# Kernel tuning notes

Measured on AMD Instinct MI355X. Metric: run time of the kernel, lower is better.

The kernel has to match this reference:

```python
import jax, jax.numpy as jnp
import numpy as np

VOC, TOPIC, EMB, BATCH = 128000, 512, 1024, 1024

def setup_inputs() -> dict:
    key = jax.random.key(0)
    k1, k2, k3 = jax.random.split(key, 3)
    x = jax.random.normal(k1, (TOPIC, BATCH), dtype=jnp.float32)
    beta0 = jax.random.normal(k2, (VOC, EMB), dtype=jnp.float32)
    beta_t = jax.random.normal(k3, (TOPIC, EMB), dtype=jnp.float32) * 0.02  # nn.init.normal_(std=0.02)
    return {"x": x, "beta0": beta0, "beta_t": beta_t, "t": 0}

def reference(x, beta0, beta_t, t):
    # w: [voc, topic] = beta0 [voc, emb] @ beta_t.T [emb, topic]
    # (the t==0 branch and else branch are identical in the source)
    w = jnp.einsum('ve,te->vt', beta0, beta_t)
    w = jax.nn.softmax(w, axis=0)  # softmax over vocab dim (dim=0)
    # out: [voc, batch]
    return jnp.einsum('vt,tb->vb', w, x)
```

## Files before the change

kernel.cpp:

```cpp
#include <hip/hip_runtime.h>

typedef _Float16 f16x8 __attribute__((ext_vector_type(8)));
typedef float    f32x4 __attribute__((ext_vector_type(4)));
typedef unsigned short u16;

#define VOC   128000
#define TOPIC 512
#define EMB   1024
#define BATCH 1024
#define ROWB  128

__device__ __forceinline__ int swz(int row, int kbyte) {
    return row * ROWB + (kbyte ^ ((row & 7) << 4));
}
__device__ __forceinline__ int xcd_swz(int bid, int nwg) {
    return (bid & 7) * (nwg >> 3) + (bid >> 3);
}
union H2U { _Float16 h; u16 u; };

#define SBAR() asm volatile("s_barrier" ::: "memory")
#define WVM0() asm volatile("s_waitcnt vmcnt(0)" ::: "memory")
#define WLG0() asm volatile("s_waitcnt lgkmcnt(0)" ::: "memory")

__global__ void cvt_betat_kernel(const float* __restrict__ betat, u16* __restrict__ bt16) {
    const size_t g = (size_t)blockIdx.x * 256 + threadIdx.x;
    const float4* src = reinterpret_cast<const float4*>(betat) + g * 2;
    float4 a = src[0], b = src[1];
    f16x8 h;
    h[0]=(_Float16)a.x; h[1]=(_Float16)a.y; h[2]=(_Float16)a.z; h[3]=(_Float16)a.w;
    h[4]=(_Float16)b.x; h[5]=(_Float16)b.y; h[6]=(_Float16)b.z; h[7]=(_Float16)b.w;
    *(reinterpret_cast<f16x8*>(bt16) + g) = h;
}

__global__ __launch_bounds__(512, 2) void gemm1_kernel(
    const float* __restrict__ beta0, const u16* __restrict__ bt16,
    u16* __restrict__ Eg, size_t TSTR, int RSTR, float* __restrict__ sg)
{
    __shared__ char lds[98304];

    const int tid  = threadIdx.x;
    const int lane = tid & 63;
    const int wid  = tid >> 6;
    const int wr = wid >> 2, wc = wid & 3;
    const int lr = lane & 15, lk = lane >> 4;
    const int srow8  = lane >> 3;
    const int schunk = ((lane & 7) ^ srow8) * 8;

    const int bid  = xcd_swz(blockIdx.x, gridDim.x);
    const int t0   = (bid & 1) * 256;
    const int tile = bid >> 1;
    const int v0   = tile * 128;

    const int arow = tid >> 2;
    const int asp  = (tid & 3) * 2;

    f32x4 acc[4][4] = {};
    float4 rA[4];

    auto loadA = [&](int kt) {
        const float4* g = reinterpret_cast<const float4*>(
            beta0 + (size_t)(v0 + arow) * EMB + kt * 64 + asp * 8);
        rA[0] = g[0]; rA[1] = g[1]; rA[2] = g[2]; rA[3] = g[3];
    };
    auto issueB = [&](int kt, int buf) {
        const u16* bsrc = bt16 + (size_t)(t0 + wid * 8 + srow8) * EMB + kt * 64 + schunk;
        char* dstb = lds + 32768 + buf * 32768;
        #pragma unroll
        for (int p = 0; p < 4; ++p)
            __builtin_amdgcn_global_load_lds(
                (const __attribute__((address_space(1))) unsigned int*)(bsrc + (size_t)p * 64 * EMB),
                (__attribute__((address_space(3))) unsigned int*)(dstb + (p * 64 + wid * 8) * ROWB),
                16, 0, 0);
    };

    issueB(0, 0);
    loadA(0);

    for (int kt = 0; kt < EMB / 64; ++kt) {
        const int cur = kt & 1;
        char* ldsA = lds + cur * 16384;
        char* ldsB = lds + 32768 + cur * 32768;

        SBAR();
        WVM0();
        {
            f16x8 h;
            h[0]=(_Float16)rA[0].x; h[1]=(_Float16)rA[0].y; h[2]=(_Float16)rA[0].z; h[3]=(_Float16)rA[0].w;
            h[4]=(_Float16)rA[1].x; h[5]=(_Float16)rA[1].y; h[6]=(_Float16)rA[1].z; h[7]=(_Float16)rA[1].w;
            *reinterpret_cast<f16x8*>(ldsA + swz(arow, asp * 16)) = h;
            f16x8 h2;
            h2[0]=(_Float16)rA[2].x; h2[1]=(_Float16)rA[2].y; h2[2]=(_Float16)rA[2].z; h2[3]=(_Float16)rA[2].w;
            h2[4]=(_Float16)rA[3].x; h2[5]=(_Float16)rA[3].y; h2[6]=(_Float16)rA[3].z; h2[7]=(_Float16)rA[3].w;
            *reinterpret_cast<f16x8*>(ldsA + swz(arow, (asp + 1) * 16)) = h2;
        }
        if (kt + 1 < EMB / 64) { issueB(kt + 1, cur ^ 1); loadA(kt + 1); }
        WLG0();
        SBAR();
        #pragma unroll
        for (int ks = 0; ks < 2; ++ks) {
            f16x8 af[4], bf[4];
            #pragma unroll
            for (int m = 0; m < 4; ++m)
                af[m] = *reinterpret_cast<const f16x8*>(ldsA + swz(wr * 64 + m * 16 + lr, ks * 64 + lk * 16));
            #pragma unroll
            for (int n = 0; n < 4; ++n)
                bf[n] = *reinterpret_cast<const f16x8*>(ldsB + swz(wc * 64 + n * 16 + lr, ks * 64 + lk * 16));
            #pragma unroll
            for (int m = 0; m < 4; ++m)
                #pragma unroll
                for (int n = 0; n < 4; ++n)
                    acc[m][n] = __builtin_amdgcn_mfma_f32_16x16x32_f16(
                        af[m], bf[n], acc[m][n], 0, 0, 0);
        }
    }

    __syncthreads();
    u16* ldsE = reinterpret_cast<u16*>(lds);
    float csum = 0.f;
    #pragma unroll
    for (int c = 0; c < 2; ++c) {
        if (wr == c) {
            #pragma unroll
            for (int m = 0; m < 4; ++m)
              #pragma unroll
              for (int n = 0; n < 4; ++n)
                #pragma unroll
                for (int r = 0; r < 4; ++r) {
                    const int row = m * 16 + lk * 4 + r;
                    const int col = wc * 64 + n * 16 + lr;
                    H2U cv; cv.h = (_Float16)__expf(acc[m][n][r]);
                    ldsE[row * 264 + col] = cv.u;
                }
        }
        __syncthreads();
        {
            const int row8 = tid >> 3, seg = tid & 7;
            const int4* srcp = reinterpret_cast<const int4*>(&ldsE[row8 * 264 + seg * 32]);
            u16* dst = Eg + tile * TSTR + (size_t)(c * 64 + row8) * RSTR + t0 + seg * 32;
            int4 v0v = srcp[0], v1v = srcp[1], v2v = srcp[2], v3v = srcp[3];
            int4* dp = reinterpret_cast<int4*>(dst);
            dp[0] = v0v; dp[1] = v1v; dp[2] = v2v; dp[3] = v3v;
        }
        if (tid < 256) {
            float s = 0.f;
            for (int r = 0; r < 64; ++r) { H2U cv; cv.u = ldsE[r * 264 + tid]; s += (float)cv.h; }
            csum += s;
        }
        __syncthreads();
    }
    if (tid < 256) atomicAdd(sg + t0 + tid, csum);
}

__global__ void xst_kernel(const float* __restrict__ x, const float* __restrict__ s,
                           u16* __restrict__ xsT)
{
    __shared__ float tile[32][33];
    const int b0 = blockIdx.x * 32, t0 = blockIdx.y * 32;
    const int tx = threadIdx.x, ty = threadIdx.y;
    tile[ty][tx] = x[(size_t)(t0 + ty) * BATCH + b0 + tx];
    __syncthreads();
    const float sc = 65536.0f / s[t0 + tx];
    H2U cv; cv.h = (_Float16)(tile[tx][ty] * sc);
    xsT[(size_t)(b0 + ty) * TOPIC + t0 + tx] = cv.u;
}

__global__ __launch_bounds__(512, 2) void gemm2a_kernel(
    const u16* __restrict__ Eg, size_t TSTR, int RSTR,
    const u16* __restrict__ xsT, float* __restrict__ out, int c0, int nch)
{
    __shared__ char lds[98304];

    const int tid  = threadIdx.x;
    const int lane = tid & 63;
    const int wid  = tid >> 6;
    const int wr = wid >> 2, wc = wid & 3;
    const int lr = lane & 15, lk = lane >> 4;
    const int srow8  = lane >> 3;
    const int schunk = ((lane & 7) ^ srow8) * 8;

    const int bid   = xcd_swz(blockIdx.x, gridDim.x);
    const int tile  = bid / nch;
    const int chunk = bid % nch;
    const int b0    = c0 + chunk * 256;
    const int v0    = tile * 128;
    const u16* Et   = Eg + tile * TSTR;

    f32x4 acc[4][4] = {};

    auto issueAB = [&](int kt, int buf) {
        const int k0 = kt * 64;
        char* dA = lds + buf * 16384;
        char* dB = lds + 32768 + buf * 32768;
        #pragma unroll
        for (int p = 0; p < 2; ++p) {
            const int rbase = p * 64 + wid * 8;
            __builtin_amdgcn_global_load_lds(
                (const __attribute__((address_space(1))) unsigned int*)
                    (Et + (size_t)(rbase + srow8) * RSTR + k0 + schunk),
                (__attribute__((address_space(3))) unsigned int*)(dA + rbase * ROWB),
                16, 0, 0);
        }
        #pragma unroll
        for (int p = 0; p < 4; ++p) {
            const int rbase = p * 64 + wid * 8;
            __builtin_amdgcn_global_load_lds(
                (const __attribute__((address_space(1))) unsigned int*)
                    (xsT + (size_t)(b0 + rbase + srow8) * TOPIC + k0 + schunk),
                (__attribute__((address_space(3))) unsigned int*)(dB + rbase * ROWB),
                16, 0, 0);
        }
    };

    issueAB(0, 0);

    for (int kt = 0; kt < TOPIC / 64; ++kt) {
        const int cur = kt & 1;
        char* ldsA = lds + cur * 16384;
        char* ldsB = lds + 32768 + cur * 32768;

        SBAR();
        WVM0();
        if (kt + 1 < TOPIC / 64) issueAB(kt + 1, cur ^ 1);
        SBAR();
        #pragma unroll
        for (int ks = 0; ks < 2; ++ks) {
            f16x8 af[4], bf[4];
            #pragma unroll
            for (int m = 0; m < 4; ++m)
                af[m] = *reinterpret_cast<const f16x8*>(ldsA + swz(wr * 64 + m * 16 + lr, ks * 64 + lk * 16));
            #pragma unroll
            for (int n = 0; n < 4; ++n)
                bf[n] = *reinterpret_cast<const f16x8*>(ldsB + swz(wc * 64 + n * 16 + lr, ks * 64 + lk * 16));
            #pragma unroll
            for (int m = 0; m < 4; ++m)
                #pragma unroll
                for (int n = 0; n < 4; ++n)
                    acc[m][n] = __builtin_amdgcn_mfma_f32_16x16x32_f16(
                        af[m], bf[n], acc[m][n], 0, 0, 0);
        }
    }

    #pragma unroll
    for (int m = 0; m < 4; ++m)
      #pragma unroll
      for (int n = 0; n < 4; ++n)
        #pragma unroll
        for (int r = 0; r < 4; ++r) {
            const int row = wr * 64 + m * 16 + lk * 4 + r;
            const int col = wc * 64 + n * 16 + lr;
            out[(size_t)(v0 + row) * BATCH + b0 + col] = acc[m][n][r] * 0x1p-16f;
        }
}

__global__ __launch_bounds__(512, 2) void gemm2b_kernel(
    const u16* __restrict__ EgBase,
    const u16* __restrict__ xsT, float* __restrict__ out)
{
    __shared__ char lds[65536];

    const int tid  = threadIdx.x;
    const int lane = tid & 63;
    const int wid  = tid >> 6;
    const int wr = wid >> 2, wc = wid & 3;
    const int lr = lane & 15, lk = lane >> 4;

    const int bid  = xcd_swz(blockIdx.x, gridDim.x);
    const int tile = bid >> 1;
    const int h    = bid & 1;
    const u16* Et  = EgBase + (size_t)tile * 262144;

    f16x8 af[2][16];
    #pragma unroll
    for (int m = 0; m < 2; ++m) {
        const int row = h * 64 + wr * 32 + m * 16 + lr;
        #pragma unroll
        for (int kb = 0; kb < 16; ++kb)
            af[m][kb] = *reinterpret_cast<const f16x8*>(
                Et + (size_t)row * 2048 + kb * 32 + lk * 8);
    }
    WVM0();
    __syncthreads();

    int4 rX[4];
    auto loadX = [&](int kt) {
        const int srow = tid >> 1;
        const int sp   = (tid & 1) * 4;
        const int4* gv = reinterpret_cast<const int4*>(
            xsT + (size_t)srow * TOPIC + kt * 64 + sp * 8);
        rX[0] = gv[0]; rX[1] = gv[1]; rX[2] = gv[2]; rX[3] = gv[3];
    };
    loadX(0);

    f32x4 acc[2][4] = {};
    for (int kt = 0; kt < 8; ++kt) {
        const int cur = kt & 1;
        char* ldsB = lds + cur * 32768;

        SBAR();
        WVM0();
        {
            const int srow = tid >> 1;
            const int sp   = (tid & 1) * 4;
            *reinterpret_cast<int4*>(ldsB + swz(srow, (sp + 0) * 16)) = rX[0];
            *reinterpret_cast<int4*>(ldsB + swz(srow, (sp + 1) * 16)) = rX[1];
            *reinterpret_cast<int4*>(ldsB + swz(srow, (sp + 2) * 16)) = rX[2];
            *reinterpret_cast<int4*>(ldsB + swz(srow, (sp + 3) * 16)) = rX[3];
        }
        if (kt + 1 < 8) loadX(kt + 1);
        WLG0();
        SBAR();
        #pragma unroll
        for (int kk = 0; kk < 2; ++kk) {
            f16x8 bf[4];
            #pragma unroll
            for (int n = 0; n < 4; ++n)
                bf[n] = *reinterpret_cast<const f16x8*>(ldsB + swz(wc * 64 + n * 16 + lr, kk * 64 + lk * 16));
            #pragma unroll
            for (int m = 0; m < 2; ++m)
                #pragma unroll
                for (int n = 0; n < 4; ++n)
                    acc[m][n] = __builtin_amdgcn_mfma_f32_16x16x32_f16(
                        af[m][kt * 2 + kk], bf[n], acc[m][n], 0, 0, 0);
        }
    }

    #pragma unroll
    for (int m = 0; m < 2; ++m)
      #pragma unroll
      for (int n = 0; n < 4; ++n)
        #pragma unroll
        for (int r = 0; r < 4; ++r) {
            const int row = h * 64 + wr * 32 + m * 16 + lk * 4 + r;
            const int col = wc * 64 + n * 16 + lr;
            out[((size_t)tile * 128 + row) * BATCH + col] = acc[m][n][r] * 0x1p-16f;
        }
}

extern "C" void kernel_launch(void* const* d_in, const int* in_sizes, int n_in,
                              void* d_out, int out_size, void* d_ws, size_t ws_size,
                              hipStream_t stream)
{
    const float* x     = (const float*)d_in[0];
    const float* beta0 = (const float*)d_in[1];
    const float* betat = (const float*)d_in[2];
    float* out = (float*)d_out;

    const size_t need_min = 4096 + (size_t)BATCH * TOPIC * 2;
    if (ws_size < need_min) return;
    float* s_g  = (float*)d_ws;
    u16*   buf1 = (u16*)((char*)d_ws + 4096);

    const size_t E_OFF = 4u * 1024u * 1024u;
    const bool big = ws_size >= E_OFF + (size_t)VOC * TOPIC * 2;

    hipMemsetAsync(d_ws, 0, 2048, stream);
    cvt_betat_kernel<<<256, 256, 0, stream>>>(betat, buf1);

    if (big) {
        u16* EgW = (u16*)((char*)d_ws + E_OFF);
        gemm1_kernel<<<2000, 512, 0, stream>>>(beta0, buf1, EgW, (size_t)128 * 512, 512, s_g);
        xst_kernel<<<dim3(BATCH / 32, TOPIC / 32), dim3(32, 32), 0, stream>>>(x, s_g, buf1);
        gemm2a_kernel<<<4000, 512, 0, stream>>>(EgW, (size_t)128 * 512, 512, buf1, out, 0, 4);
    } else {
        u16* EgO = (u16*)d_out;
        gemm1_kernel<<<2000, 512, 0, stream>>>(beta0, buf1, EgO, (size_t)262144, 2048, s_g);
        xst_kernel<<<dim3(BATCH / 32, TOPIC / 32), dim3(32, 32), 0, stream>>>(x, s_g, buf1);
        gemm2a_kernel<<<3000, 512, 0, stream>>>(EgO, (size_t)262144, 2048, buf1, out, 256, 3);
        gemm2b_kernel<<<2000, 512, 0, stream>>>(EgO, buf1, out);
    }
}
```

Baseline: 515.4 us.

## Triple-buffer LDS and prefetch two stages ahead in both GEMM kernels

Both GEMM main loops move from double buffering with a full vmcnt(0) drain each step to a three-slot LDS ring that prefetches two K-steps ahead. A partial s_waitcnt vmcnt(N) waits only for the current stage's loads. In gemm1 the fp32 A operand is held in two alternating register sets, and the loop is unrolled by two through a macro. The aim is to keep more global loads in flight and hide memory latency behind MFMA work. In exchange it uses more LDS (128KB and 144KB per block) and more registers, which could limit occupancy.

```diff
diff --git a/kernel.cpp b/kernel.cpp
--- a/kernel.cpp
+++ b/kernel.cpp
@@ -20,6 +20,8 @@
 
 #define SBAR() asm volatile("s_barrier" ::: "memory")
 #define WVM0() asm volatile("s_waitcnt vmcnt(0)" ::: "memory")
+#define WVM6() asm volatile("s_waitcnt vmcnt(6)" ::: "memory")
+#define WVM8() asm volatile("s_waitcnt vmcnt(8)" ::: "memory")
 #define WLG0() asm volatile("s_waitcnt lgkmcnt(0)" ::: "memory")
 
 __global__ void cvt_betat_kernel(const float* __restrict__ betat, u16* __restrict__ bt16) {
@@ -36,7 +38,7 @@
     const float* __restrict__ beta0, const u16* __restrict__ bt16,
     u16* __restrict__ Eg, size_t TSTR, int RSTR, float* __restrict__ sg)
 {
-    __shared__ char lds[98304];
+    __shared__ char lds[131072];
 
     const int tid  = threadIdx.x;
     const int lane = tid & 63;
@@ -55,16 +57,18 @@
     const int asp  = (tid & 3) * 2;
 
     f32x4 acc[4][4] = {};
-    float4 rA[4];
-
-    auto loadA = [&](int kt) {
-        const float4* g = reinterpret_cast<const float4*>(
-            beta0 + (size_t)(v0 + arow) * EMB + kt * 64 + asp * 8);
-        rA[0] = g[0]; rA[1] = g[1]; rA[2] = g[2]; rA[3] = g[3];
-    };
-    auto issueB = [&](int kt, int buf) {
+    float4 rAa[4], rAb[4];
+
+    const float4* aBase = reinterpret_cast<const float4*>(
+        beta0 + (size_t)(v0 + arow) * EMB);
+
+#define G1_LOADA(RA, kt) { \
+    const float4* gp = aBase + (kt) * 16 + asp * 2; \
+    RA[0] = gp[0]; RA[1] = gp[1]; RA[2] = gp[2]; RA[3] = gp[3]; }
+
+    auto issueB = [&](int kt) {
         const u16* bsrc = bt16 + (size_t)(t0 + wid * 8 + srow8) * EMB + kt * 64 + schunk;
-        char* dstb = lds + 32768 + buf * 32768;
+        char* dstb = lds + 32768 + (kt % 3) * 32768;
         #pragma unroll
         for (int p = 0; p < 4; ++p)
             __builtin_amdgcn_global_load_lds(
@@ -73,45 +77,46 @@
                 16, 0, 0);
     };
 
-    issueB(0, 0);
-    loadA(0);
-
-    for (int kt = 0; kt < EMB / 64; ++kt) {
-        const int cur = kt & 1;
-        char* ldsA = lds + cur * 16384;
-        char* ldsB = lds + 32768 + cur * 32768;
-
-        SBAR();
-        WVM0();
-        {
-            f16x8 h;
-            h[0]=(_Float16)rA[0].x; h[1]=(_Float16)rA[0].y; h[2]=(_Float16)rA[0].z; h[3]=(_Float16)rA[0].w;
-            h[4]=(_Float16)rA[1].x; h[5]=(_Float16)rA[1].y; h[6]=(_Float16)rA[1].z; h[7]=(_Float16)rA[1].w;
-            *reinterpret_cast<f16x8*>(ldsA + swz(arow, asp * 16)) = h;
-            f16x8 h2;
-            h2[0]=(_Float16)rA[2].x; h2[1]=(_Float16)rA[2].y; h2[2]=(_Float16)rA[2].z; h2[3]=(_Float16)rA[2].w;
-            h2[4]=(_Float16)rA[3].x; h2[5]=(_Float16)rA[3].y; h2[6]=(_Float16)rA[3].z; h2[7]=(_Float16)rA[3].w;
-            *reinterpret_cast<f16x8*>(ldsA + swz(arow, (asp + 1) * 16)) = h2;
-        }
-        if (kt + 1 < EMB / 64) { issueB(kt + 1, cur ^ 1); loadA(kt + 1); }
-        WLG0();
-        SBAR();
-        #pragma unroll
-        for (int ks = 0; ks < 2; ++ks) {
-            f16x8 af[4], bf[4];
-            #pragma unroll
-            for (int m = 0; m < 4; ++m)
-                af[m] = *reinterpret_cast<const f16x8*>(ldsA + swz(wr * 64 + m * 16 + lr, ks * 64 + lk * 16));
-            #pragma unroll
-            for (int n = 0; n < 4; ++n)
-                bf[n] = *reinterpret_cast<const f16x8*>(ldsB + swz(wc * 64 + n * 16 + lr, ks * 64 + lk * 16));
-            #pragma unroll
-            for (int m = 0; m < 4; ++m)
-                #pragma unroll
-                for (int n = 0; n < 4; ++n)
-                    acc[m][n] = __builtin_amdgcn_mfma_f32_16x16x32_f16(
-                        af[m], bf[n], acc[m][n], 0, 0, 0);
-        }
+    issueB(0); G1_LOADA(rAa, 0);
+    issueB(1); G1_LOADA(rAb, 1);
+
+#define G1_STEP(kt, RA) { \
+    SBAR();                        \
+    if ((kt) < 15) { WVM8(); } else { WVM0(); }   \
+    char* ldsA = lds + ((kt) & 1) * 16384; \
+    char* ldsB = lds + 32768 + ((kt) % 3) * 32768; \
+    { f16x8 h; \
+      h[0]=(_Float16)RA[0].x; h[1]=(_Float16)RA[0].y; h[2]=(_Float16)RA[0].z; h[3]=(_Float16)RA[0].w; \
+      h[4]=(_Float16)RA[1].x; h[5]=(_Float16)RA[1].y; h[6]=(_Float16)RA[1].z; h[7]=(_Float16)RA[1].w; \
+      *reinterpret_cast<f16x8*>(ldsA + swz(arow, asp * 16)) = h; \
+      f16x8 h2; \
+      h2[0]=(_Float16)RA[2].x; h2[1]=(_Float16)RA[2].y; h2[2]=(_Float16)RA[2].z; h2[3]=(_Float16)RA[2].w; \
+      h2[4]=(_Float16)RA[3].x; h2[5]=(_Float16)RA[3].y; h2[6]=(_Float16)RA[3].z; h2[7]=(_Float16)RA[3].w; \
+      *reinterpret_cast<f16x8*>(ldsA + swz(arow, (asp + 1) * 16)) = h2; } \
+    if ((kt) + 2 < 16) { issueB((kt) + 2); G1_LOADA(RA, (kt) + 2); } \
+    WLG0(); \
+    SBAR();                        \
+    _Pragma("unroll") \
+    for (int ks = 0; ks < 2; ++ks) { \
+        f16x8 af[4], bf[4]; \
+        _Pragma("unroll") \
+        for (int m = 0; m < 4; ++m) \
+            af[m] = *reinterpret_cast<const f16x8*>(ldsA + swz(wr * 64 + m * 16 + lr, ks * 64 + lk * 16)); \
+        _Pragma("unroll") \
+        for (int n = 0; n < 4; ++n) \
+            bf[n] = *reinterpret_cast<const f16x8*>(ldsB + swz(wc * 64 + n * 16 + lr, ks * 64 + lk * 16)); \
+        _Pragma("unroll") \
+        for (int m = 0; m < 4; ++m) \
+            _Pragma("unroll") \
+            for (int n = 0; n < 4; ++n) \
+                acc[m][n] = __builtin_amdgcn_mfma_f32_16x16x32_f16( \
+                    af[m], bf[n], acc[m][n], 0, 0, 0); \
+    } }
+
+    for (int k2 = 0; k2 < 8; ++k2) {
+        const int kt0 = 2 * k2;
+        G1_STEP(kt0,     rAa);
+        G1_STEP(kt0 + 1, rAb);
     }
 
     __syncthreads();
@@ -168,7 +173,7 @@
     const u16* __restrict__ Eg, size_t TSTR, int RSTR,
     const u16* __restrict__ xsT, float* __restrict__ out, int c0, int nch)
 {
-    __shared__ char lds[98304];
+    __shared__ char lds[147456];
 
     const int tid  = threadIdx.x;
     const int lane = tid & 63;
@@ -187,10 +192,10 @@
 
     f32x4 acc[4][4] = {};
 
-    auto issueAB = [&](int kt, int buf) {
+    auto issueAB = [&](int kt) {
         const int k0 = kt * 64;
-        char* dA = lds + buf * 16384;
-        char* dB = lds + 32768 + buf * 32768;
+        char* dA = lds + (kt % 3) * 16384;
+        char* dB = lds + 49152 + (kt % 3) * 32768;
         #pragma unroll
         for (int p = 0; p < 2; ++p) {
             const int rbase = p * 64 + wid * 8;
@@ -211,16 +216,16 @@
         }
     };
 
-    issueAB(0, 0);
+    issueAB(0);
+    issueAB(1);
 
     for (int kt = 0; kt < TOPIC / 64; ++kt) {
-        const int cur = kt & 1;
-        char* ldsA = lds + cur * 16384;
-        char* ldsB = lds + 32768 + cur * 32768;
+        char* ldsA = lds + (kt % 3) * 16384;
+        char* ldsB = lds + 49152 + (kt % 3) * 32768;
 
         SBAR();
-        WVM0();
-        if (kt + 1 < TOPIC / 64) issueAB(kt + 1, cur ^ 1);
+        if (kt < TOPIC / 64 - 1) { WVM6(); } else { WVM0(); }
+        if (kt + 2 < TOPIC / 64) issueAB(kt + 2);
         SBAR();
         #pragma unroll
         for (int ks = 0; ks < 2; ++ks) {
```

Measured after the change: 523.6 us. About the same (+1.6%).

## Use 256x256 tiles with interleaved LDS staging and MFMA phases in both GEMMs

Applied to the files above, without the earlier changes.

Both GEMMs now compute 256x256 output tiles per block (8x4 accumulators per wave) instead of 128x256, using 128KB double-buffered LDS. Each k-step is split into four phases that overlap global loads and LDS staging with MFMA groups, with s_setprio raised around the MFMAs. The workspace/out-buffer dual path and the register-resident gemm2b are dropped: E is always written into the output buffer, and the chunk that would overwrite it runs last. The aim is more operand reuse and fewer global reads per FLOP. The cost is that the larger LDS footprint limits residency to one block per CU, and the XCD swizzle is generalized for grid sizes that are not multiples of 8.

```diff
diff --git a/kernel.cpp b/kernel.cpp
--- a/kernel.cpp
+++ b/kernel.cpp
@@ -14,13 +14,34 @@
     return row * ROWB + (kbyte ^ ((row & 7) << 4));
 }
 __device__ __forceinline__ int xcd_swz(int bid, int nwg) {
-    return (bid & 7) * (nwg >> 3) + (bid >> 3);
+    int x = bid & 7, o = bid >> 3, q = nwg >> 3, r = nwg & 7;
+    return (x < r ? x * (q + 1) : r * (q + 1) + (x - r) * q) + o;
 }
 union H2U { _Float16 h; u16 u; };
 
 #define SBAR() asm volatile("s_barrier" ::: "memory")
 #define WVM0() asm volatile("s_waitcnt vmcnt(0)" ::: "memory")
 #define WLG0() asm volatile("s_waitcnt lgkmcnt(0)" ::: "memory")
+
+#define GLDS(SRC, DST) __builtin_amdgcn_global_load_lds( \
+    (const __attribute__((address_space(1))) unsigned int*)(SRC), \
+    (__attribute__((address_space(3))) unsigned int*)(DST), 16, 0, 0)
+
+#define RD_A(MH, KS) { _Pragma("unroll") \
+    for (int m = 0; m < 4; ++m) \
+        af[m] = *(const f16x8*)(bufA + wr * 16384 + \
+            swz((MH) * 64 + m * 16 + lr, (KS) * 64 + lk * 16)); }
+#define RD_B(KS) { _Pragma("unroll") \
+    for (int n = 0; n < 4; ++n) \
+        bf[n] = *(const f16x8*)(bufB + (wc >> 1) * 16384 + \
+            swz((wc & 1) * 64 + n * 16 + lr, (KS) * 64 + lk * 16)); }
+#define MFMA16(MH) { \
+    __builtin_amdgcn_s_setprio(1); \
+    _Pragma("unroll") for (int m = 0; m < 4; ++m) \
+    _Pragma("unroll") for (int n = 0; n < 4; ++n) \
+        acc[(MH) * 4 + m][n] = __builtin_amdgcn_mfma_f32_16x16x32_f16( \
+            af[m], bf[n], acc[(MH) * 4 + m][n], 0, 0, 0); \
+    __builtin_amdgcn_s_setprio(0); }
 
 __global__ void cvt_betat_kernel(const float* __restrict__ betat, u16* __restrict__ bt16) {
     const size_t g = (size_t)blockIdx.x * 256 + threadIdx.x;
@@ -34,9 +55,9 @@
 
 __global__ __launch_bounds__(512, 2) void gemm1_kernel(
     const float* __restrict__ beta0, const u16* __restrict__ bt16,
-    u16* __restrict__ Eg, size_t TSTR, int RSTR, float* __restrict__ sg)
-{
-    __shared__ char lds[98304];
+    u16* __restrict__ Eg, float* __restrict__ sg)
+{
+    __shared__ char lds[131072];
 
     const int tid  = threadIdx.x;
     const int lane = tid & 63;
@@ -46,80 +67,82 @@
     const int srow8  = lane >> 3;
     const int schunk = ((lane & 7) ^ srow8) * 8;
 
-    const int bid  = xcd_swz(blockIdx.x, gridDim.x);
-    const int t0   = (bid & 1) * 256;
-    const int tile = bid >> 1;
-    const int v0   = tile * 128;
-
-    const int arow = tid >> 2;
-    const int asp  = (tid & 3) * 2;
-
-    f32x4 acc[4][4] = {};
-    float4 rA[4];
-
-    auto loadA = [&](int kt) {
-        const float4* g = reinterpret_cast<const float4*>(
-            beta0 + (size_t)(v0 + arow) * EMB + kt * 64 + asp * 8);
-        rA[0] = g[0]; rA[1] = g[1]; rA[2] = g[2]; rA[3] = g[3];
-    };
-    auto issueB = [&](int kt, int buf) {
-        const u16* bsrc = bt16 + (size_t)(t0 + wid * 8 + srow8) * EMB + kt * 64 + schunk;
-        char* dstb = lds + 32768 + buf * 32768;
-        #pragma unroll
-        for (int p = 0; p < 4; ++p)
-            __builtin_amdgcn_global_load_lds(
-                (const __attribute__((address_space(1))) unsigned int*)(bsrc + (size_t)p * 64 * EMB),
-                (__attribute__((address_space(3))) unsigned int*)(dstb + (p * 64 + wid * 8) * ROWB),
-                16, 0, 0);
-    };
-
-    issueB(0, 0);
-    loadA(0);
-
-    for (int kt = 0; kt < EMB / 64; ++kt) {
-        const int cur = kt & 1;
-        char* ldsA = lds + cur * 16384;
-        char* ldsB = lds + 32768 + cur * 32768;
-
-        SBAR();
+    const int bid   = xcd_swz(blockIdx.x, gridDim.x);
+    const int tile  = bid >> 1;
+    const int chunk = bid & 1;
+    const int v0 = tile * 256, t0 = chunk * 256;
+
+    const int a_row = tid >> 1, a_kh = tid & 1;
+    const float* aRowP = beta0 + (size_t)(v0 + a_row) * EMB + a_kh * 32;
+
+    f32x4 acc[8][4] = {};
+    f16x8 af[4], bf[4];
+    float4 rA[8];
+
+    auto loadA4 = [&](int kt, int j0) {
+        const float4* g = reinterpret_cast<const float4*>(aRowP + kt * 64);
+        #pragma unroll
+        for (int j = 0; j < 4; ++j) rA[j0 + j] = g[j0 + j];
+    };
+    auto cvtA = [&](int kt1, int j0) {
+        char* dA = lds + (kt1 & 1) * 65536 + (a_row >> 7) * 16384;
+        const int rl = a_row & 127;
+        #pragma unroll
+        for (int jj = 0; jj < 2; ++jj) {
+            float4 xx = rA[j0 + jj * 2], yy = rA[j0 + jj * 2 + 1];
+            f16x8 h;
+            h[0]=(_Float16)xx.x; h[1]=(_Float16)xx.y; h[2]=(_Float16)xx.z; h[3]=(_Float16)xx.w;
+            h[4]=(_Float16)yy.x; h[5]=(_Float16)yy.y; h[6]=(_Float16)yy.z; h[7]=(_Float16)yy.w;
+            *(f16x8*)(dA + swz(rl, (a_kh * 4 + (j0 >> 1) + jj) * 16)) = h;
+        }
+    };
+    auto stageB = [&](int kt, int h) {
+        char* dstb = lds + (kt & 1) * 65536 + 32768 + h * 16384;
+        #pragma unroll
+        for (int q = 0; q < 2; ++q) {
+            const u16* s_ = bt16 + (size_t)(t0 + h * 128 + wid * 16 + q * 8 + srow8) * EMB
+                          + kt * 64 + schunk;
+            GLDS(s_, dstb + (wid * 16 + q * 8) * ROWB);
+        }
+    };
+
+    loadA4(0, 0); loadA4(0, 4);
+    stageB(0, 0); stageB(0, 1);
+    cvtA(0, 0); cvtA(0, 4);
+    WLG0();
+
+    for (int t = 0; t < 16; ++t) {
+        char* bufA = lds + (t & 1) * 65536;
+        char* bufB = bufA + 32768;
+        const bool st = (t + 1) < 16;
+
         WVM0();
-        {
-            f16x8 h;
-            h[0]=(_Float16)rA[0].x; h[1]=(_Float16)rA[0].y; h[2]=(_Float16)rA[0].z; h[3]=(_Float16)rA[0].w;
-            h[4]=(_Float16)rA[1].x; h[5]=(_Float16)rA[1].y; h[6]=(_Float16)rA[1].z; h[7]=(_Float16)rA[1].w;
-            *reinterpret_cast<f16x8*>(ldsA + swz(arow, asp * 16)) = h;
-            f16x8 h2;
-            h2[0]=(_Float16)rA[2].x; h2[1]=(_Float16)rA[2].y; h2[2]=(_Float16)rA[2].z; h2[3]=(_Float16)rA[2].w;
-            h2[4]=(_Float16)rA[3].x; h2[5]=(_Float16)rA[3].y; h2[6]=(_Float16)rA[3].z; h2[7]=(_Float16)rA[3].w;
-            *reinterpret_cast<f16x8*>(ldsA + swz(arow, (asp + 1) * 16)) = h2;
-        }
-        if (kt + 1 < EMB / 64) { issueB(kt + 1, cur ^ 1); loadA(kt + 1); }
+        SBAR();
+        RD_A(0, 0); RD_B(0);
+        if (st) { loadA4(t + 1, 0); stageB(t + 1, 0); }
+        MFMA16(0);
+        SBAR();
+        RD_A(1, 0);
+        if (st) { loadA4(t + 1, 4); stageB(t + 1, 1); }
+        MFMA16(1);
+        SBAR();
+        RD_A(0, 1); RD_B(1);
+        if (st) cvtA(t + 1, 0);
+        MFMA16(0);
+        SBAR();
+        RD_A(1, 1);
+        if (st) cvtA(t + 1, 4);
+        MFMA16(1);
         WLG0();
-        SBAR();
-        #pragma unroll
-        for (int ks = 0; ks < 2; ++ks) {
-            f16x8 af[4], bf[4];
-            #pragma unroll
-            for (int m = 0; m < 4; ++m)
-                af[m] = *reinterpret_cast<const f16x8*>(ldsA + swz(wr * 64 + m * 16 + lr, ks * 64 + lk * 16));
-            #pragma unroll
-            for (int n = 0; n < 4; ++n)
-                bf[n] = *reinterpret_cast<const f16x8*>(ldsB + swz(wc * 64 + n * 16 + lr, ks * 64 + lk * 16));
-            #pragma unroll
-            for (int m = 0; m < 4; ++m)
-                #pragma unroll
-                for (int n = 0; n < 4; ++n)
-                    acc[m][n] = __builtin_amdgcn_mfma_f32_16x16x32_f16(
-                        af[m], bf[n], acc[m][n], 0, 0, 0);
-        }
     }
 
     __syncthreads();
     u16* ldsE = reinterpret_cast<u16*>(lds);
     float csum = 0.f;
     #pragma unroll
-    for (int c = 0; c < 2; ++c) {
-        if (wr == c) {
+    for (int c = 0; c < 4; ++c) {
+        if (wr == (c >> 1)) {
+            const int mb = (c & 1) * 4;
             #pragma unroll
             for (int m = 0; m < 4; ++m)
               #pragma unroll
@@ -128,18 +151,18 @@
                 for (int r = 0; r < 4; ++r) {
                     const int row = m * 16 + lk * 4 + r;
                     const int col = wc * 64 + n * 16 + lr;
-                    H2U cv; cv.h = (_Float16)__expf(acc[m][n][r]);
+                    H2U cv; cv.h = (_Float16)__expf(acc[mb + m][n][r]);
                     ldsE[row * 264 + col] = cv.u;
                 }
         }
         __syncthreads();
         {
             const int row8 = tid >> 3, seg = tid & 7;
-            const int4* srcp = reinterpret_cast<const int4*>(&ldsE[row8 * 264 + seg * 32]);
-            u16* dst = Eg + tile * TSTR + (size_t)(c * 64 + row8) * RSTR + t0 + seg * 32;
-            int4 v0v = srcp[0], v1v = srcp[1], v2v = srcp[2], v3v = srcp[3];
+            const int4* sp = reinterpret_cast<const int4*>(&ldsE[row8 * 264 + seg * 32]);
+            u16* dst = Eg + (size_t)(v0 + c * 64 + row8) * 2048 + t0 + seg * 32;
+            int4 a0 = sp[0], a1 = sp[1], a2 = sp[2], a3 = sp[3];
             int4* dp = reinterpret_cast<int4*>(dst);
-            dp[0] = v0v; dp[1] = v1v; dp[2] = v2v; dp[3] = v3v;
+            dp[0] = a0; dp[1] = a1; dp[2] = a2; dp[3] = a3;
         }
         if (tid < 256) {
             float s = 0.f;
@@ -164,11 +187,11 @@
     xsT[(size_t)(b0 + ty) * TOPIC + t0 + tx] = cv.u;
 }
 
-__global__ __launch_bounds__(512, 2) void gemm2a_kernel(
-    const u16* __restrict__ Eg, size_t TSTR, int RSTR,
-    const u16* __restrict__ xsT, float* __restrict__ out, int c0, int nch)
-{
-    __shared__ char lds[98304];
+__global__ __launch_bounds__(512, 2) void gemm2_kernel(
+    const u16* __restrict__ Eg, const u16* __restrict__ xsT,
+    float* __restrict__ out, int c0, int nch)
+{
+    __shared__ char lds[131072];
 
     const int tid  = threadIdx.x;
     const int lane = tid & 63;
@@ -181,159 +204,68 @@
     const int bid   = xcd_swz(blockIdx.x, gridDim.x);
     const int tile  = bid / nch;
     const int chunk = bid % nch;
-    const int b0    = c0 + chunk * 256;
-    const int v0    = tile * 128;
-    const u16* Et   = Eg + tile * TSTR;
-
-    f32x4 acc[4][4] = {};
-
-    auto issueAB = [&](int kt, int buf) {
-        const int k0 = kt * 64;
-        char* dA = lds + buf * 16384;
-        char* dB = lds + 32768 + buf * 32768;
-        #pragma unroll
-        for (int p = 0; p < 2; ++p) {
-            const int rbase = p * 64 + wid * 8;
-            __builtin_amdgcn_global_load_lds(
-                (const __attribute__((address_space(1))) unsigned int*)
-                    (Et + (size_t)(rbase + srow8) * RSTR + k0 + schunk),
-                (__attribute__((address_space(3))) unsigned int*)(dA + rbase * ROWB),
-                16, 0, 0);
-        }
-        #pragma unroll
-        for (int p = 0; p < 4; ++p) {
-            const int rbase = p * 64 + wid * 8;
-            __builtin_amdgcn_global_load_lds(
-                (const __attribute__((address_space(1))) unsigned int*)
-                    (xsT + (size_t)(b0 + rbase + srow8) * TOPIC + k0 + schunk),
-                (__attribute__((address_space(3))) unsigned int*)(dB + rbase * ROWB),
-                16, 0, 0);
-        }
-    };
-
-    issueAB(0, 0);
-
-    for (int kt = 0; kt < TOPIC / 64; ++kt) {
-        const int cur = kt & 1;
-        char* ldsA = lds + cur * 16384;
-        char* ldsB = lds + 32768 + cur * 32768;
-
-        SBAR();
+    const int v0 = tile * 256, b0 = (c0 + chunk) * 256;
+
+    f32x4 acc[8][4] = {};
+    f16x8 af[4], bf[4];
+
+    auto stageA = [&](int kt, int h) {
+        char* dsta = lds + (kt & 1) * 65536 + h * 16384;
+        #pragma unroll
+        for (int q = 0; q < 2; ++q) {
+            const u16* s_ = Eg + (size_t)(v0 + h * 128 + wid * 16 + q * 8 + srow8) * 2048
+                          + kt * 64 + schunk;
+            GLDS(s_, dsta + (wid * 16 + q * 8) * ROWB);
+        }
+    };
+    auto stageB = [&](int kt, int h) {
+        char* dstb = lds + (kt & 1) * 65536 + 32768 + h * 16384;
+        #pragma unroll
+        for (int q = 0; q < 2; ++q) {
+            const u16* s_ = xsT + (size_t)(b0 + h * 128 + wid * 16 + q * 8 + srow8) * TOPIC
+                          + kt * 64 + schunk;
+            GLDS(s_, dstb + (wid * 16 + q * 8) * ROWB);
+        }
+    };
+
+    stageA(0, 0); stageA(0, 1); stageB(0, 0); stageB(0, 1);
+
+    for (int t = 0; t < 8; ++t) {
+        char* bufA = lds + (t & 1) * 65536;
+        char* bufB = bufA + 32768;
+        const bool st = (t + 1) < 8;
+
         WVM0();
-        if (kt + 1 < TOPIC / 64) issueAB(kt + 1, cur ^ 1);
-        SBAR();
-        #pragma unroll
-        for (int ks = 0; ks < 2; ++ks) {
-            f16x8 af[4], bf[4];
-            #pragma unroll
-            for (int m = 0; m < 4; ++m)
-                af[m] = *reinterpret_cast<const f16x8*>(ldsA + swz(wr * 64 + m * 16 + lr, ks * 64 + lk * 16));
-            #pragma unroll
-            for (int n = 0; n < 4; ++n)
-                bf[n] = *reinterpret_cast<const f16x8*>(ldsB + swz(wc * 64 + n * 16 + lr, ks * 64 + lk * 16));
-            #pragma unroll
-            for (int m = 0; m < 4; ++m)
-                #pragma unroll
-                for (int n = 0; n < 4; ++n)
-                    acc[m][n] = __builtin_amdgcn_mfma_f32_16x16x32_f16(
-                        af[m], bf[n], acc[m][n], 0, 0, 0);
-        }
+        SBAR();
+        RD_A(0, 0); RD_B(0);
+        if (st) stageA(t + 1, 0);
+        MFMA16(0);
+        SBAR();
+        RD_A(1, 0);
+        if (st) stageA(t + 1, 1);
+        MFMA16(1);
+        SBAR();
+        RD_A(0, 1); RD_B(1);
+        if (st) stageB(t + 1, 0);
+        MFMA16(0);
+        SBAR();
+        RD_A(1, 1);
+        if (st) stageB(t + 1, 1);
+        MFMA16(1);
     }
 
     #pragma unroll
-    for (int m = 0; m < 4; ++m)
+    for (int mh = 0; mh < 2; ++mh)
       #pragma unroll
-      for (int n = 0; n < 4; ++n)
-        #pragma unroll
-        for (int r = 0; r < 4; ++r) {
-            const int row = wr * 64 + m * 16 + lk * 4 + r;
-            const int col = wc * 64 + n * 16 + lr;
-            out[(size_t)(v0 + row) * BATCH + b0 + col] = acc[m][n][r] * 0x1p-16f;
-        }
-}
-
-__global__ __launch_bounds__(512, 2) void gemm2b_kernel(
-    const u16* __restrict__ EgBase,
-    const u16* __restrict__ xsT, float* __restrict__ out)
-{
-    __shared__ char lds[65536];
-
-    const int tid  = threadIdx.x;
-    const int lane = tid & 63;
-    const int wid  = tid >> 6;
-    const int wr = wid >> 2, wc = wid & 3;
-    const int lr = lane & 15, lk = lane >> 4;
-
-    const int bid  = xcd_swz(blockIdx.x, gridDim.x);
-    const int tile = bid >> 1;
-    const int h    = bid & 1;
-    const u16* Et  = EgBase + (size_t)tile * 262144;
-
-    f16x8 af[2][16];
-    #pragma unroll
-    for (int m = 0; m < 2; ++m) {
-        const int row = h * 64 + wr * 32 + m * 16 + lr;
-        #pragma unroll
-        for (int kb = 0; kb < 16; ++kb)
-            af[m][kb] = *reinterpret_cast<const f16x8*>(
-                Et + (size_t)row * 2048 + kb * 32 + lk * 8);
-    }
-    WVM0();
-    __syncthreads();
-
-    int4 rX[4];
-    auto loadX = [&](int kt) {
-        const int srow = tid >> 1;
-        const int sp   = (tid & 1) * 4;
-        const int4* gv = reinterpret_cast<const int4*>(
-            xsT + (size_t)srow * TOPIC + kt * 64 + sp * 8);
-        rX[0] = gv[0]; rX[1] = gv[1]; rX[2] = gv[2]; rX[3] = gv[3];
-    };
-    loadX(0);
-
-    f32x4 acc[2][4] = {};
-    for (int kt = 0; kt < 8; ++kt) {
-        const int cur = kt & 1;
-        char* ldsB = lds + cur * 32768;
-
-        SBAR();
-        WVM0();
-        {
-            const int srow = tid >> 1;
-            const int sp   = (tid & 1) * 4;
-            *reinterpret_cast<int4*>(ldsB + swz(srow, (sp + 0) * 16)) = rX[0];
-            *reinterpret_cast<int4*>(ldsB + swz(srow, (sp + 1) * 16)) = rX[1];
-            *reinterpret_cast<int4*>(ldsB + swz(srow, (sp + 2) * 16)) = rX[2];
-            *reinterpret_cast<int4*>(ldsB + swz(srow, (sp + 3) * 16)) = rX[3];
-        }
-        if (kt + 1 < 8) loadX(kt + 1);
-        WLG0();
-        SBAR();
-        #pragma unroll
-        for (int kk = 0; kk < 2; ++kk) {
-            f16x8 bf[4];
-            #pragma unroll
-            for (int n = 0; n < 4; ++n)
-                bf[n] = *reinterpret_cast<const f16x8*>(ldsB + swz(wc * 64 + n * 16 + lr, kk * 64 + lk * 16));
-            #pragma unroll
-            for (int m = 0; m < 2; ++m)
-                #pragma unroll
-                for (int n = 0; n < 4; ++n)
-                    acc[m][n] = __builtin_amdgcn_mfma_f32_16x16x32_f16(
-                        af[m][kt * 2 + kk], bf[n], acc[m][n], 0, 0, 0);
-        }
-    }
-
-    #pragma unroll
-    for (int m = 0; m < 2; ++m)
-      #pragma unroll
-      for (int n = 0; n < 4; ++n)
-        #pragma unroll
-        for (int r = 0; r < 4; ++r) {
-            const int row = h * 64 + wr * 32 + m * 16 + lk * 4 + r;
-            const int col = wc * 64 + n * 16 + lr;
-            out[((size_t)tile * 128 + row) * BATCH + col] = acc[m][n][r] * 0x1p-16f;
-        }
+      for (int m = 0; m < 4; ++m)
+        #pragma unroll
+        for (int n = 0; n < 4; ++n)
+          #pragma unroll
+          for (int r = 0; r < 4; ++r) {
+              const int row = wr * 128 + mh * 64 + m * 16 + lk * 4 + r;
+              const int col = wc * 64 + n * 16 + lr;
+              out[(size_t)(v0 + row) * BATCH + b0 + col] = acc[mh * 4 + m][n][r] * 0x1p-16f;
+          }
 }
 
 extern "C" void kernel_launch(void* const* d_in, const int* in_sizes, int n_in,
@@ -350,22 +282,14 @@
     float* s_g  = (float*)d_ws;
     u16*   buf1 = (u16*)((char*)d_ws + 4096);
 
-    const size_t E_OFF = 4u * 1024u * 1024u;
-    const bool big = ws_size >= E_OFF + (size_t)VOC * TOPIC * 2;
-
     hipMemsetAsync(d_ws, 0, 2048, stream);
     cvt_betat_kernel<<<256, 256, 0, stream>>>(betat, buf1);
 
-    if (big) {
-        u16* EgW = (u16*)((char*)d_ws + E_OFF);
-        gemm1_kernel<<<2000, 512, 0, stream>>>(beta0, buf1, EgW, (size_t)128 * 512, 512, s_g);
-        xst_kernel<<<dim3(BATCH / 32, TOPIC / 32), dim3(32, 32), 0, stream>>>(x, s_g, buf1);
-        gemm2a_kernel<<<4000, 512, 0, stream>>>(EgW, (size_t)128 * 512, 512, buf1, out, 0, 4);
-    } else {
-        u16* EgO = (u16*)d_out;
-        gemm1_kernel<<<2000, 512, 0, stream>>>(beta0, buf1, EgO, (size_t)262144, 2048, s_g);
-        xst_kernel<<<dim3(BATCH / 32, TOPIC / 32), dim3(32, 32), 0, stream>>>(x, s_g, buf1);
-        gemm2a_kernel<<<3000, 512, 0, stream>>>(EgO, (size_t)262144, 2048, buf1, out, 256, 3);
-        gemm2b_kernel<<<2000, 512, 0, stream>>>(EgO, buf1, out);
-    }
-}
+    u16* EgO = (u16*)d_out;
+    gemm1_kernel<<<1000, 512, 0, stream>>>(beta0, buf1, EgO, s_g);
+
+    xst_kernel<<<dim3(BATCH / 32, TOPIC / 32), dim3(32, 32), 0, stream>>>(x, s_g, buf1);
+
+    gemm2_kernel<<<1500, 512, 0, stream>>>(EgO, buf1, out, 1, 3);
+    gemm2_kernel<<<500,  512, 0, stream>>>(EgO, buf1, out, 0, 1);
+}
```

Result: slower. 569.5 us (+10.5%).
